# Optimization experiments

Measured on AMD Instinct MI355X. Metric: run time of the kernel, lower is better.

## Reference

```python
import jax, jax.numpy as jnp
import numpy as np
import math

EMBED = 1024
FF = 4096
HEADS = 16
HEAD = EMBED // HEADS
EPS = 1e-5


def new_gelu(x):
    c = math.sqrt(2.0 / math.pi)
    return 0.5 * x * (1.0 + jnp.tanh(c * (x + 0.044715 * x ** 3)))


def layer_norm(x, g, b):
    mu = jnp.mean(x, axis=-1, keepdims=True)
    var = jnp.var(x, axis=-1, keepdims=True)
    return (x - mu) * jax.lax.rsqrt(var + EPS) * g + b


def setup_inputs() -> dict:
    key = jax.random.key(0)
    ks = jax.random.split(key, 16)
    s = 0.02
    d = {
        'x': jax.random.normal(ks[0], (2, 2048, EMBED), jnp.float32),
        'Wq': jax.random.normal(ks[1], (EMBED, EMBED)) * s,
        'bq': jnp.zeros((EMBED,)),
        'Wk': jax.random.normal(ks[2], (EMBED, EMBED)) * s,
        'bk': jnp.zeros((EMBED,)),
        'Wv': jax.random.normal(ks[3], (EMBED, EMBED)) * s,
        'bv': jnp.zeros((EMBED,)),
        'Wp': jax.random.normal(ks[4], (EMBED, EMBED)) * s,
        'bp': jnp.zeros((EMBED,)),
        'W1': jax.random.normal(ks[5], (EMBED, FF)) * s,
        'b1': jnp.zeros((FF,)),
        'W2': jax.random.normal(ks[6], (FF, EMBED)) * s,
        'b2': jnp.zeros((EMBED,)),
        'g1': jnp.ones((EMBED,)), 'be1': jnp.zeros((EMBED,)),
        'g2': jnp.ones((EMBED,)), 'be2': jnp.zeros((EMBED,)),
    }
    return d


def reference(x, Wq, bq, Wk, bk, Wv, bv, Wp, bp, W1, b1, W2, b2, g1, be1, g2, be2):
    B, S, D = x.shape
    h = layer_norm(x, g1, be1)
    # project and split heads: [B,S,D] -> [B,H,S,Hd]
    def heads(y):
        return y.reshape(B, S, HEADS, HEAD).transpose(0, 2, 1, 3)
    Q = heads(h @ Wq + bq)
    K = heads(h @ Wk + bk)
    V = heads(h @ Wv + bv)
    att = jnp.einsum('bhqd,bhkd->bhqk', Q, K) / math.sqrt(HEAD)
    att = jax.nn.softmax(att, axis=-1)
    out = jnp.einsum('bhqk,bhkd->bhqd', att, V)
    out = out.transpose(0, 2, 1, 3).reshape(B, S, D)
    x = x + (out @ Wp + bp)  # dropout p=0 / eval -> identity
    h2 = layer_norm(x, g2, be2)
    x = x + (new_gelu(h2 @ W1 + b1) @ W2 + b2)
    return x
```

## Files before the change

kernel.cpp:

```cpp
#include <hip/hip_runtime.h>
#include <cstdint>


typedef __attribute__((ext_vector_type(8))) short short8;
typedef __attribute__((ext_vector_type(4))) float f32x4;

__device__ __forceinline__ float bf2f(unsigned short u) {
    union { unsigned int i; float f; } v; v.i = ((unsigned int)u) << 16; return v.f;
}
__device__ __forceinline__ unsigned short f2bf(float f) {
    union { float f; unsigned int i; } v; v.f = f;
    unsigned int u = v.i;
    u += 0x7fff + ((u >> 16) & 1);
    return (unsigned short)(u >> 16);
}
__device__ __forceinline__ float gelu_f(float x) {
    float u = 0.7978845608028654f * (x + 0.044715f * x * x * x);
    float t = 1.f - 2.f / (__expf(2.f * u) + 1.f);
    return 0.5f * x * (1.f + t);
}
__device__ __forceinline__ void async16(const unsigned short* gp, unsigned short* lp) {
    __builtin_amdgcn_global_load_lds(
        (__attribute__((address_space(1))) void*)(gp),
        (__attribute__((address_space(3))) void*)(lp),
        16, 0, 0);
}

__global__ __launch_bounds__(256) void ln_k(
    const float* __restrict__ x,
    const float* __restrict__ g,
    const float* __restrict__ b,
    unsigned short* __restrict__ o)
{
    const int row = blockIdx.x;
    const int tid = threadIdx.x;
    const float4 v = ((const float4*)(x + (size_t)row * 1024))[tid];
    float f0 = v.x, f1 = v.y, f2 = v.z, f3 = v.w;
    float sum = f0 + f1 + f2 + f3;
    float sq  = f0 * f0 + f1 * f1 + f2 * f2 + f3 * f3;
    for (int off = 1; off < 64; off <<= 1) {
        sum += __shfl_xor(sum, off);
        sq  += __shfl_xor(sq,  off);
    }
    __shared__ float red[8];
    int wv = tid >> 6, ln = tid & 63;
    if (ln == 0) { red[wv] = sum; red[4 + wv] = sq; }
    __syncthreads();
    sum = red[0] + red[1] + red[2] + red[3];
    sq  = red[4] + red[5] + red[6] + red[7];
    float mu  = sum * (1.0f / 1024.0f);
    float var = sq  * (1.0f / 1024.0f) - mu * mu;
    float rsd = rsqrtf(fmaxf(var, 0.f) + 1e-5f);
    const float4 gg = ((const float4*)g)[tid];
    const float4 bb = ((const float4*)b)[tid];
    unsigned short* orow = o + (size_t)row * 1024;
    orow[4 * tid + 0] = f2bf((f0 - mu) * rsd * gg.x + bb.x);
    orow[4 * tid + 1] = f2bf((f1 - mu) * rsd * gg.y + bb.y);
    orow[4 * tid + 2] = f2bf((f2 - mu) * rsd * gg.z + bb.z);
    orow[4 * tid + 3] = f2bf((f3 - mu) * rsd * gg.w + bb.w);
}

__global__ __launch_bounds__(256) void transpose_f2b(
    const float* __restrict__ in,
    unsigned short* __restrict__ out, int R, int C, int inStride)
{
    __shared__ unsigned short tile[64][70];
    const int tx = threadIdx.x & 15, ty = threadIdx.x >> 4;
    const int c0 = blockIdx.x * 64, r0 = blockIdx.y * 64;
#pragma unroll
    for (int i = 0; i < 4; ++i) {
        int r = ty + 16 * i;
        float4 v = *(const float4*)(in + (size_t)(r0 + r) * inStride + c0 + tx * 4);
        tile[r][tx * 4 + 0] = f2bf(v.x);
        tile[r][tx * 4 + 1] = f2bf(v.y);
        tile[r][tx * 4 + 2] = f2bf(v.z);
        tile[r][tx * 4 + 3] = f2bf(v.w);
    }
    __syncthreads();
#pragma unroll
    for (int i = 0; i < 4; ++i) {
        int c = ty * 4 + i;
        ushort4 o;
        o.x = tile[tx * 4 + 0][c];
        o.y = tile[tx * 4 + 1][c];
        o.z = tile[tx * 4 + 2][c];
        o.w = tile[tx * 4 + 3][c];
        *(ushort4*)(out + (size_t)(c0 + c) * R + r0 + tx * 4) = o;
    }
}

__global__ __launch_bounds__(256) void vt_k(
    const unsigned short* __restrict__ src, int stride,
    unsigned short* __restrict__ Vt)
{
    __shared__ unsigned short tile[64][70];
    const int tx = threadIdx.x & 15, ty = threadIdx.x >> 4;
    const int t0 = blockIdx.x * 64;
    const int bh = blockIdx.y;
    const int bo = (bh >> 4) * 2048;
    const int ho = (bh & 15) * 64;
    const unsigned short* s = src + (size_t)bo * stride + ho;
#pragma unroll
    for (int i = 0; i < 4; ++i) {
        int r = ty + 16 * i;
        ushort4 v = *(const ushort4*)(s + (size_t)(t0 + r) * stride + tx * 4);
        tile[r][tx * 4 + 0] = v.x;
        tile[r][tx * 4 + 1] = v.y;
        tile[r][tx * 4 + 2] = v.z;
        tile[r][tx * 4 + 3] = v.w;
    }
    __syncthreads();
    unsigned short* dst = Vt + (size_t)bh * 64 * 2048;
#pragma unroll
    for (int i = 0; i < 4; ++i) {
        int d = ty * 4 + i;
        ushort4 o;
        o.x = tile[tx * 4 + 0][d];
        o.y = tile[tx * 4 + 1][d];
        o.z = tile[tx * 4 + 2][d];
        o.w = tile[tx * 4 + 3][d];
        *(ushort4*)(dst + (size_t)d * 2048 + t0 + tx * 4) = o;
    }
}

__global__ __launch_bounds__(256) void bcat_k(
    const float* __restrict__ a, const float* __restrict__ b,
    const float* __restrict__ c, float* __restrict__ dst)
{
    int i = blockIdx.x * 256 + threadIdx.x;
    float v = (i < 1024) ? a[i] : (i < 2048) ? b[i - 1024] : c[i - 2048];
    dst[i] = v;
}

__global__ __launch_bounds__(256, 2) void gemm_bt(
    const unsigned short* __restrict__ A,
    const unsigned short* __restrict__ Bt,
    const float* __restrict__ bias,
    const float* __restrict__ res,
    void* __restrict__ C,
    int M, int N, int K, int ldb, int dogelu, int out32)
{
    __shared__ unsigned short sA[128 * 32];
    __shared__ unsigned short sB[128 * 32];
    const int tid  = threadIdx.x;
    const int wave = tid >> 6;
    const int lane = tid & 63;
    const int quad = lane >> 4;
    const int l15  = lane & 15;
    const int bm = blockIdx.y * 128;
    const int bn = blockIdx.x * 128;
    const int wM = (wave >> 1) * 64;
    const int wN = (wave & 1) * 64;

    f32x4 acc[4][4];
#pragma unroll
    for (int i = 0; i < 4; ++i)
#pragma unroll
        for (int j = 0; j < 4; ++j)
            acc[i][j] = (f32x4){0.f, 0.f, 0.f, 0.f};

    const int rowS = tid >> 2;
    const int kcS  = (tid & 3) * 8;
    const unsigned short* gA  = A  + (size_t)(bm + rowS) * K + kcS;
    const unsigned short* gA2 = gA + (size_t)64 * K;
    const unsigned short* gB  = Bt + (size_t)(bn + rowS) * ldb + kcS;
    const unsigned short* gB2 = gB + (size_t)64 * ldb;
    unsigned short* lA  = sA + tid * 8;
    unsigned short* lA2 = lA + 64 * 32;
    unsigned short* lB  = sB + tid * 8;
    unsigned short* lB2 = lB + 64 * 32;

    for (int k0 = 0; k0 < K; k0 += 32) {
        __syncthreads();
        async16(gA + k0,  lA);
        async16(gA2 + k0, lA2);
        async16(gB + k0,  lB);
        async16(gB2 + k0, lB2);
        __syncthreads();

        short8 aF[4], bF[4];
#pragma unroll
        for (int mi = 0; mi < 4; ++mi)
            aF[mi] = *(const short8*)(sA + (wM + mi * 16 + l15) * 32 + quad * 8);
#pragma unroll
        for (int ni = 0; ni < 4; ++ni)
            bF[ni] = *(const short8*)(sB + (wN + ni * 16 + l15) * 32 + quad * 8);
#pragma unroll
        for (int mi = 0; mi < 4; ++mi)
#pragma unroll
            for (int ni = 0; ni < 4; ++ni)
                acc[mi][ni] = __builtin_amdgcn_mfma_f32_16x16x32_bf16(
                    aF[mi], bF[ni], acc[mi][ni], 0, 0, 0);
    }

#pragma unroll
    for (int ni = 0; ni < 4; ++ni) {
        int col = bn + wN + ni * 16 + l15;
        float bv = bias ? bias[col] : 0.f;
#pragma unroll
        for (int mi = 0; mi < 4; ++mi) {
            int row = bm + wM + mi * 16 + quad * 4;
#pragma unroll
            for (int r = 0; r < 4; ++r) {
                float v = acc[mi][ni][r] + bv;
                if (dogelu) v = gelu_f(v);
                size_t idx = (size_t)(row + r) * N + col;
                if (res) v += res[idx];
                if (out32) ((float*)C)[idx] = v;
                else       ((unsigned short*)C)[idx] = f2bf(v);
            }
        }
    }
}

__global__ __launch_bounds__(256, 2) void gemm_bt64(
    const unsigned short* __restrict__ A,
    const unsigned short* __restrict__ Bt,
    const float* __restrict__ bias,
    const float* __restrict__ res,
    void* __restrict__ C,
    int M, int N, int K, int ldb, int dogelu, int out32)
{
    __shared__ unsigned short sA[128 * 32];
    __shared__ unsigned short sB[64 * 32];
    const int tid  = threadIdx.x;
    const int wave = tid >> 6;
    const int lane = tid & 63;
    const int quad = lane >> 4;
    const int l15  = lane & 15;
    const int bm = blockIdx.y * 128;
    const int bn = blockIdx.x * 64;
    const int wM = wave * 32;

    f32x4 acc[2][4];
#pragma unroll
    for (int i = 0; i < 2; ++i)
#pragma unroll
        for (int j = 0; j < 4; ++j)
            acc[i][j] = (f32x4){0.f, 0.f, 0.f, 0.f};

    const int rowS = tid >> 2;
    const int kcS  = (tid & 3) * 8;
    const unsigned short* gA  = A  + (size_t)(bm + rowS) * K + kcS;
    const unsigned short* gA2 = gA + (size_t)64 * K;
    const unsigned short* gB  = Bt + (size_t)(bn + rowS) * ldb + kcS;
    unsigned short* lA  = sA + tid * 8;
    unsigned short* lA2 = lA + 64 * 32;
    unsigned short* lB  = sB + tid * 8;

    for (int k0 = 0; k0 < K; k0 += 32) {
        __syncthreads();
        async16(gA + k0,  lA);
        async16(gA2 + k0, lA2);
        async16(gB + k0,  lB);
        __syncthreads();

        short8 aF[2], bF[4];
#pragma unroll
        for (int mi = 0; mi < 2; ++mi)
            aF[mi] = *(const short8*)(sA + (wM + mi * 16 + l15) * 32 + quad * 8);
#pragma unroll
        for (int ni = 0; ni < 4; ++ni)
            bF[ni] = *(const short8*)(sB + (ni * 16 + l15) * 32 + quad * 8);
#pragma unroll
        for (int mi = 0; mi < 2; ++mi)
#pragma unroll
            for (int ni = 0; ni < 4; ++ni)
                acc[mi][ni] = __builtin_amdgcn_mfma_f32_16x16x32_bf16(
                    aF[mi], bF[ni], acc[mi][ni], 0, 0, 0);
    }

#pragma unroll
    for (int ni = 0; ni < 4; ++ni) {
        int col = bn + ni * 16 + l15;
        float bv = bias ? bias[col] : 0.f;
#pragma unroll
        for (int mi = 0; mi < 2; ++mi) {
            int row = bm + wM + mi * 16 + quad * 4;
#pragma unroll
            for (int r = 0; r < 4; ++r) {
                float v = acc[mi][ni][r] + bv;
                if (dogelu) v = gelu_f(v);
                size_t idx = (size_t)(row + r) * N + col;
                if (res) v += res[idx];
                if (out32) ((float*)C)[idx] = v;
                else       ((unsigned short*)C)[idx] = f2bf(v);
            }
        }
    }
}

__global__ __launch_bounds__(256, 2) void attn_k(
    const unsigned short* __restrict__ Q,
    const unsigned short* __restrict__ K,
    const unsigned short* __restrict__ Vt,
    unsigned short* __restrict__ O, int qs)
{
    __shared__ unsigned short sQ [128 * 88];
    __shared__ unsigned short sKP[128 * 88];
    __shared__ unsigned short sVt[64 * 88];

    const int tid  = threadIdx.x;
    const int wave = tid >> 6;
    const int lane = tid & 63;
    const int quad = lane >> 4;
    const int l15  = lane & 15;
    const int qb = blockIdx.x * 128;
    const int bh = blockIdx.y;
    const int bo = (bh >> 4) * 2048;
    const int ho = (bh & 15) * 64;

    const unsigned short* Qb  = Q  + (size_t)bo * qs + ho;
    const unsigned short* Kb  = K  + (size_t)bo * qs + ho;
    const unsigned short* Vtb = Vt + (size_t)bh * 64 * 2048;

    const int rowS = tid >> 3;
    const int dcS  = (tid & 7) * 8;

#pragma unroll
    for (int r = 0; r < 4; ++r) {
        int row = r * 32 + rowS;
        short8 v = *(const short8*)(Qb + (size_t)(qb + row) * qs + dcS);
        *(short8*)(sQ + row * 88 + dcS) = v;
    }

    short8 onesF;
#pragma unroll
    for (int j = 0; j < 8; ++j) onesF[j] = (short)0x3F80;

    f32x4 accO[2][4];
    f32x4 accL[2];
#pragma unroll
    for (int mi = 0; mi < 2; ++mi) {
        accL[mi] = (f32x4){0.f, 0.f, 0.f, 0.f};
#pragma unroll
        for (int nd = 0; nd < 4; ++nd) accO[mi][nd] = (f32x4){0.f, 0.f, 0.f, 0.f};
    }

    for (int kt = 0; kt < 2048; kt += 64) {
        __syncthreads();
#pragma unroll
        for (int r = 0; r < 2; ++r) {
            int row = r * 32 + rowS;
            short8 kv = *(const short8*)(Kb + (size_t)(kt + row) * qs + dcS);
            *(short8*)(sKP + row * 88 + dcS) = kv;
            short8 vv = *(const short8*)(Vtb + (size_t)row * 2048 + kt + dcS);
            *(short8*)(sVt + row * 88 + dcS) = vv;
        }
        __syncthreads();

        f32x4 accS[2][4];
#pragma unroll
        for (int mi = 0; mi < 2; ++mi)
#pragma unroll
            for (int ni = 0; ni < 4; ++ni) accS[mi][ni] = (f32x4){0.f, 0.f, 0.f, 0.f};
#pragma unroll
        for (int ks = 0; ks < 2; ++ks) {
            short8 aQ[2], bK[4];
#pragma unroll
            for (int mi = 0; mi < 2; ++mi)
                aQ[mi] = *(const short8*)(sQ + (wave * 32 + mi * 16 + l15) * 88 + ks * 32 + quad * 8);
#pragma unroll
            for (int ni = 0; ni < 4; ++ni)
                bK[ni] = *(const short8*)(sKP + (ni * 16 + l15) * 88 + ks * 32 + quad * 8);
#pragma unroll
            for (int mi = 0; mi < 2; ++mi)
#pragma unroll
                for (int ni = 0; ni < 4; ++ni)
                    accS[mi][ni] = __builtin_amdgcn_mfma_f32_16x16x32_bf16(
                        aQ[mi], bK[ni], accS[mi][ni], 0, 0, 0);
        }
        __syncthreads();

#pragma unroll
        for (int mi = 0; mi < 2; ++mi) {
            int prow = wave * 32 + mi * 16 + quad * 4;
#pragma unroll
            for (int r = 0; r < 4; ++r) {
                float p0 = __expf(accS[mi][0][r] * 0.125f);
                float p1 = __expf(accS[mi][1][r] * 0.125f);
                float p2 = __expf(accS[mi][2][r] * 0.125f);
                float p3 = __expf(accS[mi][3][r] * 0.125f);
                sKP[(prow + r) * 88 +      l15] = f2bf(p0);
                sKP[(prow + r) * 88 + 16 + l15] = f2bf(p1);
                sKP[(prow + r) * 88 + 32 + l15] = f2bf(p2);
                sKP[(prow + r) * 88 + 48 + l15] = f2bf(p3);
            }
        }

#pragma unroll
        for (int ks = 0; ks < 2; ++ks) {
            short8 aP[2], bV[4];
#pragma unroll
            for (int mi = 0; mi < 2; ++mi)
                aP[mi] = *(const short8*)(sKP + (wave * 32 + mi * 16 + l15) * 88 + ks * 32 + quad * 8);
#pragma unroll
            for (int nd = 0; nd < 4; ++nd)
                bV[nd] = *(const short8*)(sVt + (nd * 16 + l15) * 88 + ks * 32 + quad * 8);
#pragma unroll
            for (int mi = 0; mi < 2; ++mi) {
#pragma unroll
                for (int nd = 0; nd < 4; ++nd)
                    accO[mi][nd] = __builtin_amdgcn_mfma_f32_16x16x32_bf16(
                        aP[mi], bV[nd], accO[mi][nd], 0, 0, 0);
                accL[mi] = __builtin_amdgcn_mfma_f32_16x16x32_bf16(
                    aP[mi], onesF, accL[mi], 0, 0, 0);
            }
        }
    }

#pragma unroll
    for (int mi = 0; mi < 2; ++mi)
#pragma unroll
        for (int r = 0; r < 4; ++r) {
            int row = qb + wave * 32 + mi * 16 + quad * 4 + r;
            float inv = 1.f / accL[mi][r];
#pragma unroll
            for (int nd = 0; nd < 4; ++nd)
                O[(size_t)(bo + row) * 1024 + ho + nd * 16 + l15] =
                    f2bf(accO[mi][nd][r] * inv);
        }
}

extern "C" void kernel_launch(void* const* d_in, const int* in_sizes, int n_in,
                              void* d_out, int out_size, void* d_ws, size_t ws_size,
                              hipStream_t stream)
{
    (void)in_sizes; (void)n_in; (void)out_size;
    const float* x   = (const float*)d_in[0];
    const float* Wq  = (const float*)d_in[1];
    const float* bq  = (const float*)d_in[2];
    const float* Wk  = (const float*)d_in[3];
    const float* bk  = (const float*)d_in[4];
    const float* Wv  = (const float*)d_in[5];
    const float* bv  = (const float*)d_in[6];
    const float* Wp  = (const float*)d_in[7];
    const float* bp  = (const float*)d_in[8];
    const float* W1  = (const float*)d_in[9];
    const float* b1  = (const float*)d_in[10];
    const float* W2  = (const float*)d_in[11];
    const float* b2  = (const float*)d_in[12];
    const float* g1  = (const float*)d_in[13];
    const float* be1 = (const float*)d_in[14];
    const float* g2  = (const float*)d_in[15];
    const float* be2 = (const float*)d_in[16];
    float* out = (float*)d_out;

    char* ws = (char*)d_ws;
    char* dob = (char*)d_out;
    const size_t MB = 1024 * 1024;

    if (ws_size >= 40 * MB) {
        unsigned short* hb    = (unsigned short*)dob;
        unsigned short* WTqkv = (unsigned short*)(dob + 8 * MB);
        float*          bcat  = (float*)(dob + 14 * MB);
        unsigned short* QKV   = (unsigned short*)ws;
        unsigned short* att   = (unsigned short*)(ws + 24 * MB);
        unsigned short* Vt    = (unsigned short*)(ws + 32 * MB);
        unsigned short* WTp   = (unsigned short*)(ws + 32 * MB);
        unsigned short* h2    = (unsigned short*)ws;
        unsigned short* WT1   = (unsigned short*)(ws + 8 * MB);
        unsigned short* WT2   = (unsigned short*)(ws + 16 * MB);
        unsigned short* act   = (unsigned short*)(ws + 24 * MB);

        ln_k<<<4096, 256, 0, stream>>>(x, g1, be1, hb);
        transpose_f2b<<<dim3(16, 16), 256, 0, stream>>>(Wq, WTqkv,               1024, 1024, 1024);
        transpose_f2b<<<dim3(16, 16), 256, 0, stream>>>(Wk, WTqkv + 1024 * 1024, 1024, 1024, 1024);
        transpose_f2b<<<dim3(16, 16), 256, 0, stream>>>(Wv, WTqkv + 2048 * 1024, 1024, 1024, 1024);
        bcat_k<<<12, 256, 0, stream>>>(bq, bk, bv, bcat);
        gemm_bt<<<dim3(24, 32), 256, 0, stream>>>(hb, WTqkv, bcat, nullptr, QKV,
                                                  4096, 3072, 1024, 1024, 0, 0);
        vt_k<<<dim3(32, 32), 256, 0, stream>>>(QKV + 2048, 3072, Vt);
        attn_k<<<dim3(16, 32), 256, 0, stream>>>(QKV, QKV + 1024, Vt, att, 3072);
        transpose_f2b<<<dim3(16, 16), 256, 0, stream>>>(Wp, WTp, 1024, 1024, 1024);
        gemm_bt64<<<dim3(16, 32), 256, 0, stream>>>(att, WTp, bp, x, out,
                                                    4096, 1024, 1024, 1024, 0, 1);
        ln_k<<<4096, 256, 0, stream>>>(out, g2, be2, h2);
        transpose_f2b<<<dim3(64, 16), 256, 0, stream>>>(W1, WT1, 1024, 4096, 4096);
        transpose_f2b<<<dim3(16, 64), 256, 0, stream>>>(W2, WT2, 4096, 1024, 1024);
        for (int c = 0; c < 2; ++c) {
            gemm_bt<<<dim3(16, 32), 256, 0, stream>>>(h2, WT1 + (size_t)c * 2048 * 1024,
                                                      b1 + c * 2048, nullptr, act,
                                                      4096, 2048, 1024, 1024, 1, 0);
            gemm_bt64<<<dim3(16, 32), 256, 0, stream>>>(act, WT2 + (size_t)c * 2048,
                                                        c == 0 ? b2 : nullptr, out, out,
                                                        4096, 1024, 2048, 4096, 0, 1);
        }
    } else {
        unsigned short* Qw  = (unsigned short*)(ws);
        unsigned short* Kw  = (unsigned short*)(ws + 8 * MB);
        unsigned short* Vw  = (unsigned short*)(ws + 16 * MB);
        unsigned short* hb  = (unsigned short*)dob;
        unsigned short* WTq = (unsigned short*)(dob + 8 * MB);
        unsigned short* VtF = (unsigned short*)(dob + 8 * MB);
        unsigned short* att = Qw;
        unsigned short* WTb = Kw;
        unsigned short* h2  = Vw;
        unsigned short* act = Qw;

        ln_k<<<4096, 256, 0, stream>>>(x, g1, be1, hb);
        transpose_f2b<<<dim3(16, 16), 256, 0, stream>>>(Wq, WTq, 1024, 1024, 1024);
        gemm_bt<<<dim3(8, 32), 256, 0, stream>>>(hb, WTq, bq, nullptr, Qw, 4096, 1024, 1024, 1024, 0, 0);
        transpose_f2b<<<dim3(16, 16), 256, 0, stream>>>(Wk, WTq, 1024, 1024, 1024);
        gemm_bt<<<dim3(8, 32), 256, 0, stream>>>(hb, WTq, bk, nullptr, Kw, 4096, 1024, 1024, 1024, 0, 0);
        transpose_f2b<<<dim3(16, 16), 256, 0, stream>>>(Wv, WTq, 1024, 1024, 1024);
        gemm_bt<<<dim3(8, 32), 256, 0, stream>>>(hb, WTq, bv, nullptr, Vw, 4096, 1024, 1024, 1024, 0, 0);
        vt_k<<<dim3(32, 32), 256, 0, stream>>>(Vw, 1024, VtF);
        attn_k<<<dim3(16, 32), 256, 0, stream>>>(Qw, Kw, VtF, att, 1024);
        transpose_f2b<<<dim3(16, 16), 256, 0, stream>>>(Wp, WTb, 1024, 1024, 1024);
        gemm_bt64<<<dim3(16, 32), 256, 0, stream>>>(att, WTb, bp, x, out, 4096, 1024, 1024, 1024, 0, 1);
        ln_k<<<4096, 256, 0, stream>>>(out, g2, be2, h2);
        for (int c = 0; c < 4; ++c) {
            transpose_f2b<<<dim3(16, 16), 256, 0, stream>>>(W1 + c * 1024, WTb, 1024, 1024, 4096);
            gemm_bt64<<<dim3(16, 32), 256, 0, stream>>>(h2, WTb, b1 + c * 1024, nullptr, act,
                                                        4096, 1024, 1024, 1024, 1, 0);
            unsigned short* WT2c = WTb + 1024 * 1024;
            transpose_f2b<<<dim3(16, 16), 256, 0, stream>>>(W2 + (size_t)c * 1024 * 1024, WT2c,
                                                            1024, 1024, 1024);
            gemm_bt64<<<dim3(16, 32), 256, 0, stream>>>(act, WT2c, c == 0 ? b2 : nullptr,
                                                        out, out, 4096, 1024, 1024, 1024, 0, 1);
        }
    }
}
```

Before: 435.6 us.

## Merge prep kernels into combined launches and double K-step per GEMM barrier

The layernorm, weight-transpose and bias-concat launches are folded into two multi-role kernels that dispatch on block index, which cuts the number of kernel launches and lets the small transposes run alongside the layernorm blocks. Both GEMM kernels now load a 64-wide K slice (two 32-wide halves) per pair of barriers and run two MFMA sub-steps per iteration, halving barrier and sync overhead per K. This doubles LDS use per GEMM block, which may reduce occupancy, and the loads are still not overlapped with compute.

```diff
diff --git a/kernel.cpp b/kernel.cpp
--- a/kernel.cpp
+++ b/kernel.cpp
@@ -26,13 +26,11 @@
         16, 0, 0);
 }
 
-__global__ __launch_bounds__(256) void ln_k(
-    const float* __restrict__ x,
-    const float* __restrict__ g,
-    const float* __restrict__ b,
-    unsigned short* __restrict__ o)
-{
-    const int row = blockIdx.x;
+__device__ __forceinline__ void ln_dev(
+    const float* __restrict__ x, const float* __restrict__ g,
+    const float* __restrict__ b, unsigned short* __restrict__ o,
+    int row, float* red)
+{
     const int tid = threadIdx.x;
     const float4 v = ((const float4*)(x + (size_t)row * 1024))[tid];
     float f0 = v.x, f1 = v.y, f2 = v.z, f3 = v.w;
@@ -42,7 +40,6 @@
         sum += __shfl_xor(sum, off);
         sq  += __shfl_xor(sq,  off);
     }
-    __shared__ float red[8];
     int wv = tid >> 6, ln = tid & 63;
     if (ln == 0) { red[wv] = sum; red[4 + wv] = sq; }
     __syncthreads();
@@ -60,32 +57,104 @@
     orow[4 * tid + 3] = f2bf((f3 - mu) * rsd * gg.w + bb.w);
 }
 
-__global__ __launch_bounds__(256) void transpose_f2b(
-    const float* __restrict__ in,
-    unsigned short* __restrict__ out, int R, int C, int inStride)
-{
-    __shared__ unsigned short tile[64][70];
+__device__ __forceinline__ void transpose_dev(
+    const float* __restrict__ in, unsigned short* __restrict__ out,
+    int R, int C, int inStride, int bx, int by, unsigned short* tile )
+{
     const int tx = threadIdx.x & 15, ty = threadIdx.x >> 4;
-    const int c0 = blockIdx.x * 64, r0 = blockIdx.y * 64;
+    const int c0 = bx * 64, r0 = by * 64;
 #pragma unroll
     for (int i = 0; i < 4; ++i) {
         int r = ty + 16 * i;
         float4 v = *(const float4*)(in + (size_t)(r0 + r) * inStride + c0 + tx * 4);
-        tile[r][tx * 4 + 0] = f2bf(v.x);
-        tile[r][tx * 4 + 1] = f2bf(v.y);
-        tile[r][tx * 4 + 2] = f2bf(v.z);
-        tile[r][tx * 4 + 3] = f2bf(v.w);
+        tile[r * 70 + tx * 4 + 0] = f2bf(v.x);
+        tile[r * 70 + tx * 4 + 1] = f2bf(v.y);
+        tile[r * 70 + tx * 4 + 2] = f2bf(v.z);
+        tile[r * 70 + tx * 4 + 3] = f2bf(v.w);
     }
     __syncthreads();
 #pragma unroll
     for (int i = 0; i < 4; ++i) {
         int c = ty * 4 + i;
         ushort4 o;
-        o.x = tile[tx * 4 + 0][c];
-        o.y = tile[tx * 4 + 1][c];
-        o.z = tile[tx * 4 + 2][c];
-        o.w = tile[tx * 4 + 3][c];
+        o.x = tile[(tx * 4 + 0) * 70 + c];
+        o.y = tile[(tx * 4 + 1) * 70 + c];
+        o.z = tile[(tx * 4 + 2) * 70 + c];
+        o.w = tile[(tx * 4 + 3) * 70 + c];
         *(ushort4*)(out + (size_t)(c0 + c) * R + r0 + tx * 4) = o;
+    }
+}
+
+__global__ __launch_bounds__(256) void ln_k(
+    const float* __restrict__ x, const float* __restrict__ g,
+    const float* __restrict__ b, unsigned short* __restrict__ o)
+{
+    __shared__ float red[8];
+    ln_dev(x, g, b, o, blockIdx.x, red);
+}
+__global__ __launch_bounds__(256) void transpose_f2b(
+    const float* __restrict__ in, unsigned short* __restrict__ out,
+    int R, int C, int inStride)
+{
+    __shared__ unsigned short tile[64 * 70];
+    transpose_dev(in, out, R, C, inStride, blockIdx.x, blockIdx.y, tile);
+}
+__global__ __launch_bounds__(256) void bcat_k(
+    const float* __restrict__ a, const float* __restrict__ b,
+    const float* __restrict__ c, float* __restrict__ dst)
+{
+    int i = blockIdx.x * 256 + threadIdx.x;
+    float v = (i < 1024) ? a[i] : (i < 2048) ? b[i - 1024] : c[i - 2048];
+    dst[i] = v;
+}
+
+__global__ __launch_bounds__(256) void prep1_k(
+    const float* __restrict__ x,
+    const float* __restrict__ g1, const float* __restrict__ be1,
+    const float* __restrict__ Wq, const float* __restrict__ Wk,
+    const float* __restrict__ Wv,
+    const float* __restrict__ bq, const float* __restrict__ bk,
+    const float* __restrict__ bv,
+    unsigned short* __restrict__ hb,
+    unsigned short* __restrict__ WTqkv,
+    float* __restrict__ bcat)
+{
+    __shared__ unsigned short smem[64 * 70];
+    const int b = blockIdx.x;
+    if (b < 4096) {
+        ln_dev(x, g1, be1, hb, b, (float*)smem);
+    } else if (b < 4096 + 768) {
+        int t = b - 4096;
+        int w = t >> 8;
+        int tt = t & 255;
+        const float* W = (w == 0) ? Wq : (w == 1) ? Wk : Wv;
+        transpose_dev(W, WTqkv + (size_t)w * 1024 * 1024,
+                      1024, 1024, 1024, tt & 15, tt >> 4, smem);
+    } else {
+        int i = (b - 4096 - 768) * 256 + threadIdx.x;
+        float v = (i < 1024) ? bq[i] : (i < 2048) ? bk[i - 1024] : bv[i - 2048];
+        bcat[i] = v;
+    }
+}
+
+__global__ __launch_bounds__(256) void prep2_k(
+    const float* __restrict__ x1,
+    const float* __restrict__ g2, const float* __restrict__ be2,
+    const float* __restrict__ W1, const float* __restrict__ W2,
+    unsigned short* __restrict__ h2,
+    unsigned short* __restrict__ WT1,
+    unsigned short* __restrict__ WT2)
+{
+    __shared__ unsigned short smem[64 * 70];
+    const int b = blockIdx.x;
+    if (b < 4096) {
+        ln_dev(x1, g2, be2, h2, b, (float*)smem);
+    } else if (b < 4096 + 1024) {
+        int t = b - 4096;
+        transpose_dev(W1, WT1, 1024, 4096, 4096, t & 63, t >> 6, smem);
+    } else {
+        int t = b - 4096 - 1024;
+        transpose_dev(W2, WT2, 4096, 1024, 1024, t & 15, t >> 4, smem);
     }
 }
 
@@ -123,15 +192,6 @@
     }
 }
 
-__global__ __launch_bounds__(256) void bcat_k(
-    const float* __restrict__ a, const float* __restrict__ b,
-    const float* __restrict__ c, float* __restrict__ dst)
-{
-    int i = blockIdx.x * 256 + threadIdx.x;
-    float v = (i < 1024) ? a[i] : (i < 2048) ? b[i - 1024] : c[i - 2048];
-    dst[i] = v;
-}
-
 __global__ __launch_bounds__(256, 2) void gemm_bt(
     const unsigned short* __restrict__ A,
     const unsigned short* __restrict__ Bt,
@@ -140,8 +200,8 @@
     void* __restrict__ C,
     int M, int N, int K, int ldb, int dogelu, int out32)
 {
-    __shared__ unsigned short sA[128 * 32];
-    __shared__ unsigned short sB[128 * 32];
+    __shared__ unsigned short sA[2 * 128 * 32];
+    __shared__ unsigned short sB[2 * 128 * 32];
     const int tid  = threadIdx.x;
     const int wave = tid >> 6;
     const int lane = tid & 63;
@@ -170,27 +230,34 @@
     unsigned short* lB  = sB + tid * 8;
     unsigned short* lB2 = lB + 64 * 32;
 
-    for (int k0 = 0; k0 < K; k0 += 32) {
-        __syncthreads();
-        async16(gA + k0,  lA);
-        async16(gA2 + k0, lA2);
-        async16(gB + k0,  lB);
-        async16(gB2 + k0, lB2);
-        __syncthreads();
-
-        short8 aF[4], bF[4];
-#pragma unroll
-        for (int mi = 0; mi < 4; ++mi)
-            aF[mi] = *(const short8*)(sA + (wM + mi * 16 + l15) * 32 + quad * 8);
-#pragma unroll
-        for (int ni = 0; ni < 4; ++ni)
-            bF[ni] = *(const short8*)(sB + (wN + ni * 16 + l15) * 32 + quad * 8);
-#pragma unroll
-        for (int mi = 0; mi < 4; ++mi)
+    for (int k0 = 0; k0 < K; k0 += 64) {
+        __syncthreads();
+        async16(gA + k0,       lA);
+        async16(gA2 + k0,      lA2);
+        async16(gA + k0 + 32,  lA + 4096);
+        async16(gA2 + k0 + 32, lA2 + 4096);
+        async16(gB + k0,       lB);
+        async16(gB2 + k0,      lB2);
+        async16(gB + k0 + 32,  lB + 4096);
+        async16(gB2 + k0 + 32, lB2 + 4096);
+        __syncthreads();
+
+#pragma unroll
+        for (int p = 0; p < 2; ++p) {
+            short8 aF[4], bF[4];
+#pragma unroll
+            for (int mi = 0; mi < 4; ++mi)
+                aF[mi] = *(const short8*)(sA + p * 4096 + (wM + mi * 16 + l15) * 32 + quad * 8);
 #pragma unroll
             for (int ni = 0; ni < 4; ++ni)
-                acc[mi][ni] = __builtin_amdgcn_mfma_f32_16x16x32_bf16(
-                    aF[mi], bF[ni], acc[mi][ni], 0, 0, 0);
+                bF[ni] = *(const short8*)(sB + p * 4096 + (wN + ni * 16 + l15) * 32 + quad * 8);
+#pragma unroll
+            for (int mi = 0; mi < 4; ++mi)
+#pragma unroll
+                for (int ni = 0; ni < 4; ++ni)
+                    acc[mi][ni] = __builtin_amdgcn_mfma_f32_16x16x32_bf16(
+                        aF[mi], bF[ni], acc[mi][ni], 0, 0, 0);
+        }
     }
 
 #pragma unroll
@@ -221,8 +288,8 @@
     void* __restrict__ C,
     int M, int N, int K, int ldb, int dogelu, int out32)
 {
-    __shared__ unsigned short sA[128 * 32];
-    __shared__ unsigned short sB[64 * 32];
+    __shared__ unsigned short sA[2 * 128 * 32];
+    __shared__ unsigned short sB[2 * 64 * 32];
     const int tid  = threadIdx.x;
     const int wave = tid >> 6;
     const int lane = tid & 63;
@@ -248,26 +315,32 @@
     unsigned short* lA2 = lA + 64 * 32;
     unsigned short* lB  = sB + tid * 8;
 
-    for (int k0 = 0; k0 < K; k0 += 32) {
-        __syncthreads();
-        async16(gA + k0,  lA);
-        async16(gA2 + k0, lA2);
-        async16(gB + k0,  lB);
-        __syncthreads();
-
-        short8 aF[2], bF[4];
-#pragma unroll
-        for (int mi = 0; mi < 2; ++mi)
-            aF[mi] = *(const short8*)(sA + (wM + mi * 16 + l15) * 32 + quad * 8);
-#pragma unroll
-        for (int ni = 0; ni < 4; ++ni)
-            bF[ni] = *(const short8*)(sB + (ni * 16 + l15) * 32 + quad * 8);
-#pragma unroll
-        for (int mi = 0; mi < 2; ++mi)
+    for (int k0 = 0; k0 < K; k0 += 64) {
+        __syncthreads();
+        async16(gA + k0,       lA);
+        async16(gA2 + k0,      lA2);
+        async16(gA + k0 + 32,  lA + 4096);
+        async16(gA2 + k0 + 32, lA2 + 4096);
+        async16(gB + k0,       lB);
+        async16(gB + k0 + 32,  lB + 2048);
+        __syncthreads();
+
+#pragma unroll
+        for (int p = 0; p < 2; ++p) {
+            short8 aF[2], bF[4];
+#pragma unroll
+            for (int mi = 0; mi < 2; ++mi)
+                aF[mi] = *(const short8*)(sA + p * 4096 + (wM + mi * 16 + l15) * 32 + quad * 8);
 #pragma unroll
             for (int ni = 0; ni < 4; ++ni)
-                acc[mi][ni] = __builtin_amdgcn_mfma_f32_16x16x32_bf16(
-                    aF[mi], bF[ni], acc[mi][ni], 0, 0, 0);
+                bF[ni] = *(const short8*)(sB + p * 2048 + (ni * 16 + l15) * 32 + quad * 8);
+#pragma unroll
+            for (int mi = 0; mi < 2; ++mi)
+#pragma unroll
+                for (int ni = 0; ni < 4; ++ni)
+                    acc[mi][ni] = __builtin_amdgcn_mfma_f32_16x16x32_bf16(
+                        aF[mi], bF[ni], acc[mi][ni], 0, 0, 0);
+        }
     }
 
 #pragma unroll
@@ -463,11 +536,8 @@
         unsigned short* WT2   = (unsigned short*)(ws + 16 * MB);
         unsigned short* act   = (unsigned short*)(ws + 24 * MB);
 
-        ln_k<<<4096, 256, 0, stream>>>(x, g1, be1, hb);
-        transpose_f2b<<<dim3(16, 16), 256, 0, stream>>>(Wq, WTqkv,               1024, 1024, 1024);
-        transpose_f2b<<<dim3(16, 16), 256, 0, stream>>>(Wk, WTqkv + 1024 * 1024, 1024, 1024, 1024);
-        transpose_f2b<<<dim3(16, 16), 256, 0, stream>>>(Wv, WTqkv + 2048 * 1024, 1024, 1024, 1024);
-        bcat_k<<<12, 256, 0, stream>>>(bq, bk, bv, bcat);
+        prep1_k<<<4096 + 768 + 12, 256, 0, stream>>>(
+            x, g1, be1, Wq, Wk, Wv, bq, bk, bv, hb, WTqkv, bcat);
         gemm_bt<<<dim3(24, 32), 256, 0, stream>>>(hb, WTqkv, bcat, nullptr, QKV,
                                                   4096, 3072, 1024, 1024, 0, 0);
         vt_k<<<dim3(32, 32), 256, 0, stream>>>(QKV + 2048, 3072, Vt);
@@ -475,9 +545,7 @@
         transpose_f2b<<<dim3(16, 16), 256, 0, stream>>>(Wp, WTp, 1024, 1024, 1024);
         gemm_bt64<<<dim3(16, 32), 256, 0, stream>>>(att, WTp, bp, x, out,
                                                     4096, 1024, 1024, 1024, 0, 1);
-        ln_k<<<4096, 256, 0, stream>>>(out, g2, be2, h2);
-        transpose_f2b<<<dim3(64, 16), 256, 0, stream>>>(W1, WT1, 1024, 4096, 4096);
-        transpose_f2b<<<dim3(16, 64), 256, 0, stream>>>(W2, WT2, 4096, 1024, 1024);
+        prep2_k<<<4096 + 2048, 256, 0, stream>>>(out, g2, be2, W1, W2, h2, WT1, WT2);
         for (int c = 0; c < 2; ++c) {
             gemm_bt<<<dim3(16, 32), 256, 0, stream>>>(h2, WT1 + (size_t)c * 2048 * 1024,
                                                       b1 + c * 2048, nullptr, act,
```

Result: faster. 396.5 us (-9.0%).
